# Kernel optimization log

Measured on AMD Instinct MI355X. Metric: run time of the kernel, lower is better.

The kernel has to match this reference:

```python
import jax, jax.numpy as jnp
import numpy as np

N, D_IN, D_OUT = 16384, 64, 64
AVG_DEG = 32.0
L2_EPS = 1e-12  # torch F.normalize default eps


def setup_inputs() -> dict:
    key = jax.random.key(0)
    kx, ka, kw, kb = jax.random.split(key, 4)
    X = jax.random.normal(kx, (N, D_IN), dtype=jnp.float32)
    # binary adjacency with avg degree ~AVG_DEG (module treats adj as 0/1 mask)
    adj = (jax.random.uniform(ka, (N, N)) < (AVG_DEG / N)).astype(jnp.float32)
    # nn.Linear(2*D_IN, D_OUT): store W as (2*D_IN, D_OUT) for x @ W + b
    bound = 1.0 / np.sqrt(2 * D_IN)
    W = jax.random.uniform(kw, (2 * D_IN, D_OUT), dtype=jnp.float32, minval=-bound, maxval=bound)
    b = jax.random.uniform(kb, (D_OUT,), dtype=jnp.float32, minval=-bound, maxval=bound)
    return {"X": X, "adj": adj, "W": W, "b": b}


def reference(X, adj, W, b):
    # eval-mode mean aggregation: h_neigh = (adj + I) @ X / clamp(rowsum(adj + I), 1)
    # (adj + I) @ X == adj @ X + X, avoiding materializing the NxN identity.
    deg = jnp.clip(jnp.sum(adj, axis=1, keepdims=True) + 1.0, 1.0, None)  # (N,1)
    h_neigh = (adj @ X + X) / deg                                          # (N,D)
    concat = jnp.concatenate([X, h_neigh], axis=1)                         # (N,2D)
    z = concat @ W + b                                                     # (N,O)
    out = jax.nn.relu(z)
    norm = jnp.linalg.norm(out, axis=1, keepdims=True)
    return out / jnp.maximum(norm, L2_EPS)
```

## Files before the change

### kernel.cpp

```cpp
#include <hip/hip_runtime.h>
#include <stdint.h>


#define NROWS    16384
#define DDIM     64
#define MAXCHUNK 256
#define NBLOCKS  4096
#define PIPE     8

typedef uint32_t u32x4 __attribute__((ext_vector_type(4)));

__global__ __launch_bounds__(256, 6) void sage_fused(
    const float* __restrict__ X,
    const float* __restrict__ adj,
    const float* __restrict__ W,
    const float* __restrict__ bias,
    float* __restrict__ out)
{
    __shared__ int   slist[4][MAXCHUNK];
    __shared__ float scat[4][2 * DDIM];

    const int tid  = threadIdx.x;
    const int lane = tid & 63;
    const int w    = tid >> 6;
    const int row  = blockIdx.x * 4 + w;

    const float bv = bias[lane];

    const int start = ((row * 7 + (row >> 4)) & 15) * 4;
    const u32x4* rowp = reinterpret_cast<const u32x4*>(adj + (size_t)row * NROWS);

    u32x4 buf[PIPE];
#pragma unroll
    for (int i = 0; i < PIPE; ++i)
        buf[i] = rowp[((start + i) & 63) * 64 + lane];

    int cnt = 0;
#pragma unroll 1
    for (int so = 0; so < 64; so += PIPE) {
#pragma unroll
        for (int i = 0; i < PIPE; ++i) {
            const int g = (start + so + i) & 63;
            const u32x4 vv = buf[i];
            const bool nz = (vv.x | vv.y | vv.z | vv.w) != 0;
            const uint64_t bal = __ballot(nz);
            if (bal) {
                const uint32_t m = ((vv.x >> 29) & 1u) | ((vv.y >> 28) & 2u)
                                 | ((vv.z >> 27) & 4u) | ((vv.w >> 26) & 8u);
                const int prefix = __builtin_amdgcn_mbcnt_hi(
                    (uint32_t)(bal >> 32),
                    __builtin_amdgcn_mbcnt_lo((uint32_t)bal, 0));
                if (nz) {
                    const int pos = cnt + prefix;
                    if (pos < MAXCHUNK)
                        slist[w][pos] = (((g << 6) + lane) << 4) | (int)m;
                }
                cnt += (int)__popcll(bal);
            }
            if (so + PIPE < 64)
                buf[i] = rowp[((start + so + i + PIPE) & 63) * 64 + lane];
        }
    }
    __builtin_amdgcn_wave_barrier();

    const int cn = (cnt < MAXCHUNK) ? cnt : MAXCHUNK;

    float acc = 0.0f;
    int nnz = 0;
    for (int k = 0; k < cn; ++k) {
        const int e  = slist[w][k];
        const int ci = e >> 4;
        const uint32_t m = e & 15u;
        nnz += __popc(m);
        const float* xb = X + (size_t)ci * 4 * DDIM + lane;
        if (m & 1u) acc += xb[0 * DDIM];
        if (m & 2u) acc += xb[1 * DDIM];
        if (m & 4u) acc += xb[2 * DDIM];
        if (m & 8u) acc += xb[3 * DDIM];
    }

    const float xi = X[(size_t)row * DDIM + lane];
    const float h  = (acc + xi) / ((float)nnz + 1.0f);
    scat[w][lane]        = xi;
    scat[w][DDIM + lane] = h;
    __builtin_amdgcn_wave_barrier();

    float z0 = bv, z1 = 0.0f, z2 = 0.0f, z3 = 0.0f;
#pragma unroll 8
    for (int kk = 0; kk < 2 * DDIM; kk += 4) {
        z0 = fmaf(scat[w][kk + 0], W[(kk + 0) * DDIM + lane], z0);
        z1 = fmaf(scat[w][kk + 1], W[(kk + 1) * DDIM + lane], z1);
        z2 = fmaf(scat[w][kk + 2], W[(kk + 2) * DDIM + lane], z2);
        z3 = fmaf(scat[w][kk + 3], W[(kk + 3) * DDIM + lane], z3);
    }
    float z = (z0 + z1) + (z2 + z3);
    z = fmaxf(z, 0.0f);

    float s2 = z * z;
#pragma unroll
    for (int off = 32; off >= 1; off >>= 1) s2 += __shfl_xor(s2, off);
    const float inv = 1.0f / fmaxf(sqrtf(s2), 1e-12f);
    out[(size_t)row * DDIM + lane] = z * inv;
}

extern "C" void kernel_launch(void* const* d_in, const int* in_sizes, int n_in,
                              void* d_out, int out_size, void* d_ws, size_t ws_size,
                              hipStream_t stream) {
    const float* X   = (const float*)d_in[0];
    const float* adj = (const float*)d_in[1];
    const float* W   = (const float*)d_in[2];
    const float* b   = (const float*)d_in[3];
    float* out = (float*)d_out;
    sage_fused<<<NBLOCKS, 256, 0, stream>>>(X, adj, W, b, out);
}
```

Before: 1.342 ms.

## Split adjacency scan into bitmap compression pass and separate aggregation kernel

Splits the fused kernel in two. A streaming kernel first compresses the dense float adjacency into a bit mask in the workspace, with each wave handling four strided spans and double-buffered loads. The aggregation kernel then reads the compact bitmap per row instead of the full 64 KB float row, which decouples the bandwidth-bound scan from the gather and matmul work. The cost is an extra launch, a workspace write and read, and the sign-bit trick still assumes the adjacency values are exactly 0 or 1.

```diff
diff --git a/kernel.cpp b/kernel.cpp
--- a/kernel.cpp
+++ b/kernel.cpp
@@ -5,17 +5,59 @@
 #define NROWS    16384
 #define DDIM     64
 #define MAXCHUNK 256
-#define NBLOCKS  4096
-#define PIPE     8
+#define PA_BLOCKS 8192
+#define PB_BLOCKS 4096
+#define PA_WAVES ((size_t)PA_BLOCKS * 4)
+#define SPANS    ((size_t)1 << 17)
 
 typedef uint32_t u32x4 __attribute__((ext_vector_type(4)));
 
-__global__ __launch_bounds__(256, 6) void sage_fused(
-    const float* __restrict__ X,
-    const float* __restrict__ adj,
-    const float* __restrict__ W,
-    const float* __restrict__ bias,
-    float* __restrict__ out)
+__device__ __forceinline__ void ld_span(const u32x4* __restrict__ p, size_t s,
+                                        int lane, u32x4 b[8]) {
+#pragma unroll
+    for (int j = 0; j < 8; ++j) b[j] = p[s * 512 + j * 64 + lane];
+}
+
+__device__ __forceinline__ void st_span(uint32_t* __restrict__ bm, size_t s,
+                                        int lane, const u32x4 b[8]) {
+    uint32_t m = 0;
+#pragma unroll
+    for (int j = 0; j < 8; ++j) {
+        const u32x4 v = b[j];
+        const uint32_t nib = ((v.x >> 29) & 1u) | ((v.y >> 28) & 2u)
+                           | ((v.z >> 27) & 4u) | ((v.w >> 26) & 8u);
+        m |= nib << (4 * j);
+    }
+    bm[s * 64 + lane] = m;
+}
+
+__global__ __launch_bounds__(256, 4) void adj_to_bitmap(
+    const float* __restrict__ adj, uint32_t* __restrict__ bm)
+{
+    const int    lane = threadIdx.x & 63;
+    const size_t wv   = ((size_t)blockIdx.x * 256 + threadIdx.x) >> 6;
+    const u32x4* p    = reinterpret_cast<const u32x4*>(adj);
+
+    const size_t s0 = wv,                 s1 = wv + PA_WAVES,
+                 s2 = wv + 2 * PA_WAVES,  s3 = wv + 3 * PA_WAVES;
+
+    u32x4 A[8], B[8];
+    ld_span(p, s0, lane, A);
+    ld_span(p, s1, lane, B);
+    st_span(bm, s0, lane, A);
+    ld_span(p, s2, lane, A);
+    st_span(bm, s1, lane, B);
+    ld_span(p, s3, lane, B);
+    st_span(bm, s2, lane, A);
+    st_span(bm, s3, lane, B);
+}
+
+__global__ __launch_bounds__(256, 4) void sage_agg(
+    const float*    __restrict__ X,
+    const uint32_t* __restrict__ bm,
+    const float*    __restrict__ W,
+    const float*    __restrict__ bias,
+    float*          __restrict__ out)
 {
     __shared__ int   slist[4][MAXCHUNK];
     __shared__ float scat[4][2 * DDIM];
@@ -27,38 +69,29 @@
 
     const float bv = bias[lane];
 
-    const int start = ((row * 7 + (row >> 4)) & 15) * 4;
-    const u32x4* rowp = reinterpret_cast<const u32x4*>(adj + (size_t)row * NROWS);
-
-    u32x4 buf[PIPE];
+    uint32_t dw[8];
 #pragma unroll
-    for (int i = 0; i < PIPE; ++i)
-        buf[i] = rowp[((start + i) & 63) * 64 + lane];
+    for (int sp = 0; sp < 8; ++sp)
+        dw[sp] = bm[((size_t)row * 8 + sp) * 64 + lane];
 
     int cnt = 0;
 #pragma unroll 1
-    for (int so = 0; so < 64; so += PIPE) {
+    for (int sp = 0; sp < 8; ++sp) {
 #pragma unroll
-        for (int i = 0; i < PIPE; ++i) {
-            const int g = (start + so + i) & 63;
-            const u32x4 vv = buf[i];
-            const bool nz = (vv.x | vv.y | vv.z | vv.w) != 0;
-            const uint64_t bal = __ballot(nz);
+        for (int j = 0; j < 8; ++j) {
+            const uint32_t nib = (dw[sp] >> (4 * j)) & 15u;
+            const uint64_t bal = __ballot(nib != 0u);
             if (bal) {
-                const uint32_t m = ((vv.x >> 29) & 1u) | ((vv.y >> 28) & 2u)
-                                 | ((vv.z >> 27) & 4u) | ((vv.w >> 26) & 8u);
                 const int prefix = __builtin_amdgcn_mbcnt_hi(
                     (uint32_t)(bal >> 32),
                     __builtin_amdgcn_mbcnt_lo((uint32_t)bal, 0));
-                if (nz) {
+                if (nib) {
                     const int pos = cnt + prefix;
                     if (pos < MAXCHUNK)
-                        slist[w][pos] = (((g << 6) + lane) << 4) | (int)m;
+                        slist[w][pos] = ((sp * 512 + j * 64 + lane) << 4) | (int)nib;
                 }
                 cnt += (int)__popcll(bal);
             }
-            if (so + PIPE < 64)
-                buf[i] = rowp[((start + so + i + PIPE) & 63) * 64 + lane];
         }
     }
     __builtin_amdgcn_wave_barrier();
@@ -111,5 +144,9 @@
     const float* W   = (const float*)d_in[2];
     const float* b   = (const float*)d_in[3];
     float* out = (float*)d_out;
-    sage_fused<<<NBLOCKS, 256, 0, stream>>>(X, adj, W, b, out);
+
+    uint32_t* bm = (uint32_t*)d_ws;
+
+    adj_to_bitmap<<<PA_BLOCKS, 256, 0, stream>>>(adj, bm);
+    sage_agg<<<PB_BLOCKS, 256, 0, stream>>>(X, bm, W, b, out);
 }
```

Result: slower. 1.392 ms (+3.7%).
